# Kernel optimization log

Hardware: AMD Instinct MI355X
Metric: run time of the kernel (lower is better)

## Reference

```python
import jax, jax.numpy as jnp
import numpy as np

N_NODES = 100000
N_EDGES = 1600000
D_IN = 32
D_OUT = 64


def setup_inputs() -> dict:
    key = jax.random.key(0)
    ks = jax.random.split(key, 6)
    x = jax.random.normal(ks[0], (N_NODES, D_IN), dtype=jnp.float32)
    edge_row = jax.random.randint(ks[1], (N_EDGES,), 0, N_NODES, dtype=jnp.int32)
    edge_col = jax.random.randint(ks[2], (N_EDGES,), 0, N_NODES, dtype=jnp.int32)
    edge_val = jax.random.uniform(ks[3], (N_EDGES,), dtype=jnp.float32)
    W = jax.random.normal(ks[4], (D_IN, D_OUT), dtype=jnp.float32) * (1.0 / np.sqrt(D_IN))
    b = jax.random.normal(ks[5], (D_OUT,), dtype=jnp.float32) * 0.01
    return {"x": x, "edge_row": edge_row, "edge_col": edge_col,
            "edge_val": edge_val, "W": W, "b": b, "k": 4}


def _spmm(edge_row, edge_col, edge_val, x, n_nodes):
    # out[i] = sum_{e: row[e]==i} val[e] * x[col[e]]  (sparse adj @ x)
    gathered = edge_val[:, None] * x[edge_col]  # [E, D]
    return jax.ops.segment_sum(gathered, edge_row, num_segments=n_nodes)


def reference(x, edge_row, edge_col, edge_val, W, b, k):
    # k-hop propagation: x <- A @ x, repeated k times (k is a static Python int)
    for _ in range(k):
        x = _spmm(edge_row, edge_col, edge_val, x, N_NODES)
    # final dense linear: x @ W + b
    return x @ W + b
```

## Files before the change

### kernel.cpp

```cpp
#include <hip/hip_runtime.h>
#include <hip/hip_fp16.h>

#define N_NODES 100000
#define N_EDGES 1600000
#define D_IN 32
#define D_OUT 64

#define RPB 200
#define NBKT 500
#define CAP 4608
#define EPT 16
#define SCT 256
#define EPB (EPT * SCT)
#define SBLOCKS ((N_EDGES + EPB - 1) / EPB)
#define N2 (N_NODES * D_IN / 2)
#define CVT_BLOCKS ((N2 + 255) / 256)
#define NGRP (N_NODES / 4)

#define COL_BITS 17
#define COL_MASK ((1u << COL_BITS) - 1u)
#define VAL_SCALE 32767.0f
#define VAL_INV (1.0f / 32767.0f)

typedef unsigned int uv2 __attribute__((ext_vector_type(2)));
typedef unsigned int uv4 __attribute__((ext_vector_type(4)));

__global__ void init_bcur(int* __restrict__ bcur) {
    int i = threadIdx.x;
    if (i < NBKT) bcur[i] = i * CAP;
}

__global__ void scatter_chunks(const int* __restrict__ erow,
                               const int* __restrict__ ecol,
                               const float* __restrict__ eval_,
                               int* __restrict__ bcur,
                               int2* __restrict__ staged,
                               const float2* __restrict__ xf,
                               unsigned int* __restrict__ xh) {
    if (blockIdx.x >= SBLOCKS) {
        int i = (blockIdx.x - SBLOCKS) * blockDim.x + threadIdx.x;
        if (i < N2) {
            float2 f = xf[i];
            __half2 h = __floats2half2_rn(f.x, f.y);
            xh[i] = *(unsigned int*)&h;
        }
        return;
    }
    __shared__ int h[NBKT];
    __shared__ int cb[NBKT];
    for (int i = threadIdx.x; i < NBKT; i += blockDim.x) h[i] = 0;
    __syncthreads();
    int base = blockIdx.x * EPB;
    unsigned pk[EPT]; float val[EPT]; int brk[EPT];
#pragma unroll
    for (int k = 0; k < EPT; ++k) {
        int e = base + k * SCT + threadIdx.x;
        if (e < N_EDGES) {
            int r = __builtin_nontemporal_load(&erow[e]);
            int c = __builtin_nontemporal_load(&ecol[e]);
            float v = __builtin_nontemporal_load(&eval_[e]);
            int b = r / RPB;
            int rl = r - b * RPB;
            int rank = atomicAdd(&h[b], 1);
            pk[k] = ((unsigned)rl << COL_BITS) | (unsigned)c;
            val[k] = v;
            brk[k] = b | (rank << 9);
        } else brk[k] = -1;
    }
    __syncthreads();
    for (int i = threadIdx.x; i < NBKT; i += blockDim.x) {
        int c = h[i];
        if (c) cb[i] = atomicAdd(&bcur[i], c);
    }
    __syncthreads();
#pragma unroll
    for (int k = 0; k < EPT; ++k) {
        if (brk[k] >= 0) {
            int b = brk[k] & 511;
            int rank = brk[k] >> 9;
            int2 p; p.x = (int)pk[k]; p.y = __float_as_int(val[k]);
            staged[cb[b] + rank] = p;
        }
    }
}

__global__ void sort_bucket(const int* __restrict__ bcur,
                            const int2* __restrict__ staged,
                            unsigned int* __restrict__ epack,
                            int2* __restrict__ row_rng) {
    __shared__ int hist[RPB];
    __shared__ int offs[RPB];
    __shared__ int cur[RPB];
    int b = blockIdx.x;
    int s0 = b * CAP, s1 = bcur[b];
    for (int i = threadIdx.x; i < RPB; i += blockDim.x) hist[i] = 0;
    __syncthreads();
    for (int e = s0 + threadIdx.x; e < s1; e += blockDim.x) {
        unsigned w = (unsigned)staged[e].x;
        atomicAdd(&hist[w >> COL_BITS], 1);
    }
    __syncthreads();
    if (threadIdx.x == 0) {
        int run = 0;
        for (int i = 0; i < RPB; ++i) {
            offs[i] = run;
            run += (hist[i] + 7) & ~7;
        }
    }
    __syncthreads();
    int r0 = b * RPB;
    for (int i = threadIdx.x; i < RPB; i += blockDim.x) {
        int st = s0 + offs[i];
        int2 rr; rr.x = st; rr.y = st + ((hist[i] + 7) & ~7);
        row_rng[r0 + i] = rr;
        cur[i] = offs[i];
    }
    __syncthreads();
    for (int e = s0 + threadIdx.x; e < s1; e += blockDim.x) {
        int2 p = staged[e];
        unsigned w = (unsigned)p.x;
        int rl = (int)(w >> COL_BITS);
        int pos = atomicAdd(&cur[rl], 1);
        float v = __int_as_float(p.y);
        unsigned q = (unsigned)(int)(v * VAL_SCALE + 0.5f);
        epack[s0 + pos] = (q << COL_BITS) | (w & COL_MASK);
    }
    __syncthreads();
    for (int i = threadIdx.x; i < RPB; i += blockDim.x) {
        int end = offs[i] + ((hist[i] + 7) & ~7);
        for (int k = cur[i]; k < end; ++k) epack[s0 + k] = 0u;
    }
}

template <int HOP>
__global__ void __launch_bounds__(256, 8)
spmm_hop(const int2* __restrict__ row_rng,
         const uv4* __restrict__ epack4,
         const uv2* __restrict__ xin,
         uv2* __restrict__ xout) {
    int lane = threadIdx.x & 63;
    int wave = threadIdx.x >> 6;
    int qt = lane >> 4;
    int g  = (lane >> 3) & 1;
    int j  = lane & 7;
    int r = (blockIdx.x * 4 + wave) * 4 + qt;
    int2 pe = row_rng[r];
    int p0 = pe.x, p1 = pe.y;
    float4 a0 = {0.f,0.f,0.f,0.f}, a1 = {0.f,0.f,0.f,0.f};
    float4 a2 = {0.f,0.f,0.f,0.f}, a3 = {0.f,0.f,0.f,0.f};
    uv4 q = epack4[(p0 >> 2) + g];
    for (int eb = p0; eb < p1; eb += 8) {
        uv4 qn = epack4[((eb + 8) >> 2) + g];
        unsigned q0 = q.x, q1 = q.y, q2 = q.z, q3 = q.w;
        uv2 w0 = xin[(q0 & COL_MASK) * 8 + j];
        uv2 w1 = xin[(q1 & COL_MASK) * 8 + j];
        uv2 w2 = xin[(q2 & COL_MASK) * 8 + j];
        uv2 w3 = xin[(q3 & COL_MASK) * 8 + j];
        float v0 = (float)(q0 >> COL_BITS) * VAL_INV;
        float v1 = (float)(q1 >> COL_BITS) * VAL_INV;
        float v2 = (float)(q2 >> COL_BITS) * VAL_INV;
        float v3 = (float)(q3 >> COL_BITS) * VAL_INV;
        unsigned w0x = w0.x, w0y = w0.y, w1x = w1.x, w1y = w1.y;
        unsigned w2x = w2.x, w2y = w2.y, w3x = w3.x, w3y = w3.y;
        float2 f0a = __half22float2(*(__half2*)&w0x), f0b = __half22float2(*(__half2*)&w0y);
        float2 f1a = __half22float2(*(__half2*)&w1x), f1b = __half22float2(*(__half2*)&w1y);
        float2 f2a = __half22float2(*(__half2*)&w2x), f2b = __half22float2(*(__half2*)&w2y);
        float2 f3a = __half22float2(*(__half2*)&w3x), f3b = __half22float2(*(__half2*)&w3y);
        a0.x += v0 * f0a.x; a0.y += v0 * f0a.y; a0.z += v0 * f0b.x; a0.w += v0 * f0b.y;
        a1.x += v1 * f1a.x; a1.y += v1 * f1a.y; a1.z += v1 * f1b.x; a1.w += v1 * f1b.y;
        a2.x += v2 * f2a.x; a2.y += v2 * f2a.y; a2.z += v2 * f2b.x; a2.w += v2 * f2b.y;
        a3.x += v3 * f3a.x; a3.y += v3 * f3a.y; a3.z += v3 * f3b.x; a3.w += v3 * f3b.y;
        q = qn;
    }
    float4 acc;
    acc.x = (a0.x + a1.x) + (a2.x + a3.x);
    acc.y = (a0.y + a1.y) + (a2.y + a3.y);
    acc.z = (a0.z + a1.z) + (a2.z + a3.z);
    acc.w = (a0.w + a1.w) + (a2.w + a3.w);
    acc.x += __shfl_xor(acc.x, 8, 64);
    acc.y += __shfl_xor(acc.y, 8, 64);
    acc.z += __shfl_xor(acc.z, 8, 64);
    acc.w += __shfl_xor(acc.w, 8, 64);
    if (g == 0) {
        __half2 o0 = __floats2half2_rn(acc.x, acc.y);
        __half2 o1 = __floats2half2_rn(acc.z, acc.w);
        uv2 w;
        w.x = *(unsigned int*)&o0;
        w.y = *(unsigned int*)&o1;
        xout[r * 8 + j] = w;
    }
}

__global__ void linear_bias(const uv4* __restrict__ xin,
                            const float* __restrict__ W,
                            const float* __restrict__ b,
                            float* __restrict__ out) {
    __shared__ float sW[D_IN * D_OUT];
    __shared__ float sb[D_OUT];
    for (int i = threadIdx.x; i < D_IN * D_OUT; i += blockDim.x) sW[i] = W[i];
    if (threadIdx.x < D_OUT) sb[threadIdx.x] = b[threadIdx.x];
    __syncthreads();

    int sub = threadIdx.x >> 6;
    int j = threadIdx.x & 63;
    for (int grp = blockIdx.x; grp < NGRP; grp += gridDim.x) {
        int r = grp * 4 + sub;
        const uv4* xr4 = xin + (size_t)r * 4;
        float acc = sb[j];
#pragma unroll
        for (int qd = 0; qd < 4; ++qd) {
            uv4 v = xr4[qd];
            unsigned vw[4] = {v.x, v.y, v.z, v.w};
#pragma unroll
            for (int w = 0; w < 4; ++w) {
                float2 f = __half22float2(*(__half2*)&vw[w]);
                int d = 8 * qd + 2 * w;
                acc += f.x * sW[d * D_OUT + j] + f.y * sW[(d + 1) * D_OUT + j];
            }
        }
        out[r * D_OUT + j] = acc;
    }
}

extern "C" void kernel_launch(void* const* d_in, const int* in_sizes, int n_in,
                              void* d_out, int out_size, void* d_ws, size_t ws_size,
                              hipStream_t stream) {
    const float* x     = (const float*)d_in[0];
    const int*   erow  = (const int*)d_in[1];
    const int*   ecol  = (const int*)d_in[2];
    const float* eval_ = (const float*)d_in[3];
    const float* W     = (const float*)d_in[4];
    const float* b     = (const float*)d_in[5];
    float* out = (float*)d_out;

    unsigned int* xh0 = (unsigned int*)d_ws;
    unsigned int* xh1 = xh0 + (size_t)N2;
    int* bcur = (int*)(xh1 + (size_t)N2);
    int2* row_rng = (int2*)(bcur + 512);
    int2* staged = (int2*)(row_rng + N_NODES);
    unsigned int* epack = (unsigned int*)(staged + (size_t)NBKT * CAP);

    const int threads = 256;

    init_bcur<<<1, 512, 0, stream>>>(bcur);
    scatter_chunks<<<SBLOCKS + CVT_BLOCKS, SCT, 0, stream>>>(
        erow, ecol, eval_, bcur, staged, (const float2*)x, xh0);
    sort_bucket<<<NBKT, threads, 0, stream>>>(bcur, staged, epack, row_rng);

    const int sblocks = N_NODES / 16;
    spmm_hop<0><<<sblocks, threads, 0, stream>>>(row_rng, (const uv4*)epack,
                                                 (const uv2*)xh0, (uv2*)xh1);
    spmm_hop<1><<<sblocks, threads, 0, stream>>>(row_rng, (const uv4*)epack,
                                                 (const uv2*)xh1, (uv2*)xh0);
    spmm_hop<2><<<sblocks, threads, 0, stream>>>(row_rng, (const uv4*)epack,
                                                 (const uv2*)xh0, (uv2*)xh1);
    spmm_hop<3><<<sblocks, threads, 0, stream>>>(row_rng, (const uv4*)epack,
                                                 (const uv2*)xh1, (uv2*)xh0);

    linear_bias<<<2048, 256, 0, stream>>>((const uv4*)xh0, W, b, out);
}
```

Baseline: 226.8 us.

## Software-pipeline SpMM feature gathers and parallelize bucket offset scan

In the SpMM hop kernel, the gathers of x rows for the next 8-edge chunk are now issued before the FMAs of the current chunk run. This double-buffers both the packed edge words and the gathered half2 features, so gather latency overlaps with arithmetic. The sort_bucket kernel also replaces a single-thread serial prefix sum over 200 row counts with a 256-thread Hillis-Steele scan in shared memory. The trade-offs are higher register pressure under launch_bounds(256,8). The first chunk is also processed unconditionally, which would give wrong results for a row with no edges.

```diff
diff --git a/kernel.cpp b/kernel.cpp
--- a/kernel.cpp
+++ b/kernel.cpp
@@ -89,34 +89,41 @@
                             unsigned int* __restrict__ epack,
                             int2* __restrict__ row_rng) {
     __shared__ int hist[RPB];
+    __shared__ int scan[256];
     __shared__ int offs[RPB];
     __shared__ int cur[RPB];
     int b = blockIdx.x;
+    int t = threadIdx.x;
     int s0 = b * CAP, s1 = bcur[b];
-    for (int i = threadIdx.x; i < RPB; i += blockDim.x) hist[i] = 0;
-    __syncthreads();
-    for (int e = s0 + threadIdx.x; e < s1; e += blockDim.x) {
+    for (int i = t; i < RPB; i += blockDim.x) hist[i] = 0;
+    __syncthreads();
+    for (int e = s0 + t; e < s1; e += blockDim.x) {
         unsigned w = (unsigned)staged[e].x;
         atomicAdd(&hist[w >> COL_BITS], 1);
     }
     __syncthreads();
-    if (threadIdx.x == 0) {
-        int run = 0;
-        for (int i = 0; i < RPB; ++i) {
-            offs[i] = run;
-            run += (hist[i] + 7) & ~7;
-        }
-    }
+    int myv = (t < RPB) ? ((hist[t] + 7) & ~7) : 0;
+    scan[t] = myv;
+    __syncthreads();
+#pragma unroll
+    for (int off = 1; off < 256; off <<= 1) {
+        int v = 0;
+        if (t >= off) v = scan[t - off];
+        __syncthreads();
+        if (t >= off) scan[t] += v;
+        __syncthreads();
+    }
+    if (t < RPB) offs[t] = scan[t] - myv;
     __syncthreads();
     int r0 = b * RPB;
-    for (int i = threadIdx.x; i < RPB; i += blockDim.x) {
+    for (int i = t; i < RPB; i += blockDim.x) {
         int st = s0 + offs[i];
         int2 rr; rr.x = st; rr.y = st + ((hist[i] + 7) & ~7);
         row_rng[r0 + i] = rr;
         cur[i] = offs[i];
     }
     __syncthreads();
-    for (int e = s0 + threadIdx.x; e < s1; e += blockDim.x) {
+    for (int e = s0 + t; e < s1; e += blockDim.x) {
         int2 p = staged[e];
         unsigned w = (unsigned)p.x;
         int rl = (int)(w >> COL_BITS);
@@ -126,11 +133,29 @@
         epack[s0 + pos] = (q << COL_BITS) | (w & COL_MASK);
     }
     __syncthreads();
-    for (int i = threadIdx.x; i < RPB; i += blockDim.x) {
+    for (int i = t; i < RPB; i += blockDim.x) {
         int end = offs[i] + ((hist[i] + 7) & ~7);
         for (int k = cur[i]; k < end; ++k) epack[s0 + k] = 0u;
     }
 }
+
+#define FMA8(qq, u0, u1, u2, u3)                                              \
+    {                                                                         \
+        float v0 = (float)(qq.x >> COL_BITS) * VAL_INV;                       \
+        float v1 = (float)(qq.y >> COL_BITS) * VAL_INV;                       \
+        float v2 = (float)(qq.z >> COL_BITS) * VAL_INV;                       \
+        float v3 = (float)(qq.w >> COL_BITS) * VAL_INV;                       \
+        unsigned x0 = u0.x, y0 = u0.y, x1 = u1.x, y1 = u1.y;                  \
+        unsigned x2 = u2.x, y2 = u2.y, x3 = u3.x, y3 = u3.y;                  \
+        float2 f0a = __half22float2(*(__half2*)&x0), f0b = __half22float2(*(__half2*)&y0); \
+        float2 f1a = __half22float2(*(__half2*)&x1), f1b = __half22float2(*(__half2*)&y1); \
+        float2 f2a = __half22float2(*(__half2*)&x2), f2b = __half22float2(*(__half2*)&y2); \
+        float2 f3a = __half22float2(*(__half2*)&x3), f3b = __half22float2(*(__half2*)&y3); \
+        a0.x += v0 * f0a.x; a0.y += v0 * f0a.y; a0.z += v0 * f0b.x; a0.w += v0 * f0b.y; \
+        a1.x += v1 * f1a.x; a1.y += v1 * f1a.y; a1.z += v1 * f1b.x; a1.w += v1 * f1b.y; \
+        a2.x += v2 * f2a.x; a2.y += v2 * f2a.y; a2.z += v2 * f2b.x; a2.w += v2 * f2b.y; \
+        a3.x += v3 * f3a.x; a3.y += v3 * f3a.y; a3.z += v3 * f3b.x; a3.w += v3 * f3b.y; \
+    }
 
 template <int HOP>
 __global__ void __launch_bounds__(256, 8)
@@ -148,30 +173,23 @@
     int p0 = pe.x, p1 = pe.y;
     float4 a0 = {0.f,0.f,0.f,0.f}, a1 = {0.f,0.f,0.f,0.f};
     float4 a2 = {0.f,0.f,0.f,0.f}, a3 = {0.f,0.f,0.f,0.f};
-    uv4 q = epack4[(p0 >> 2) + g];
-    for (int eb = p0; eb < p1; eb += 8) {
-        uv4 qn = epack4[((eb + 8) >> 2) + g];
-        unsigned q0 = q.x, q1 = q.y, q2 = q.z, q3 = q.w;
-        uv2 w0 = xin[(q0 & COL_MASK) * 8 + j];
-        uv2 w1 = xin[(q1 & COL_MASK) * 8 + j];
-        uv2 w2 = xin[(q2 & COL_MASK) * 8 + j];
-        uv2 w3 = xin[(q3 & COL_MASK) * 8 + j];
-        float v0 = (float)(q0 >> COL_BITS) * VAL_INV;
-        float v1 = (float)(q1 >> COL_BITS) * VAL_INV;
-        float v2 = (float)(q2 >> COL_BITS) * VAL_INV;
-        float v3 = (float)(q3 >> COL_BITS) * VAL_INV;
-        unsigned w0x = w0.x, w0y = w0.y, w1x = w1.x, w1y = w1.y;
-        unsigned w2x = w2.x, w2y = w2.y, w3x = w3.x, w3y = w3.y;
-        float2 f0a = __half22float2(*(__half2*)&w0x), f0b = __half22float2(*(__half2*)&w0y);
-        float2 f1a = __half22float2(*(__half2*)&w1x), f1b = __half22float2(*(__half2*)&w1y);
-        float2 f2a = __half22float2(*(__half2*)&w2x), f2b = __half22float2(*(__half2*)&w2y);
-        float2 f3a = __half22float2(*(__half2*)&w3x), f3b = __half22float2(*(__half2*)&w3y);
-        a0.x += v0 * f0a.x; a0.y += v0 * f0a.y; a0.z += v0 * f0b.x; a0.w += v0 * f0b.y;
-        a1.x += v1 * f1a.x; a1.y += v1 * f1a.y; a1.z += v1 * f1b.x; a1.w += v1 * f1b.y;
-        a2.x += v2 * f2a.x; a2.y += v2 * f2a.y; a2.z += v2 * f2b.x; a2.w += v2 * f2b.y;
-        a3.x += v3 * f3a.x; a3.y += v3 * f3a.y; a3.z += v3 * f3b.x; a3.w += v3 * f3b.y;
-        q = qn;
-    }
+    uv4 qc = epack4[(p0 >> 2) + g];
+    uv2 w0 = xin[(qc.x & COL_MASK) * 8 + j];
+    uv2 w1 = xin[(qc.y & COL_MASK) * 8 + j];
+    uv2 w2 = xin[(qc.z & COL_MASK) * 8 + j];
+    uv2 w3 = xin[(qc.w & COL_MASK) * 8 + j];
+    uv4 qn = epack4[((p0 + 8) >> 2) + g];
+    for (int eb = p0 + 8; eb < p1; eb += 8) {
+        uv4 qf = epack4[((eb + 8) >> 2) + g];
+        uv2 n0 = xin[(qn.x & COL_MASK) * 8 + j];
+        uv2 n1 = xin[(qn.y & COL_MASK) * 8 + j];
+        uv2 n2 = xin[(qn.z & COL_MASK) * 8 + j];
+        uv2 n3 = xin[(qn.w & COL_MASK) * 8 + j];
+        FMA8(qc, w0, w1, w2, w3);
+        qc = qn; qn = qf;
+        w0 = n0; w1 = n1; w2 = n2; w3 = n3;
+    }
+    FMA8(qc, w0, w1, w2, w3);
     float4 acc;
     acc.x = (a0.x + a1.x) + (a2.x + a3.x);
     acc.y = (a0.y + a1.y) + (a2.y + a3.y);
```

Measured after the change: 218.6 us. 1.04x faster.
